# Kernel optimization log

Hardware: AMD Instinct MI355X
Metric: run time of the kernel (lower is better)

The kernel has to match this reference:

```python
import jax, jax.numpy as jnp
import numpy as np

SHAPES = [(100, 100), (50, 50), (25, 25), (13, 13)]
EMBED, HEADS, LEVELS, POINTS = 256, 8, 4, 4
DH = EMBED // HEADS


def setup_inputs() -> dict:
    key = jax.random.key(0)
    ks = jax.random.split(key, 12)
    bs, nq = 4, 10000
    nv = sum(h * w for h, w in SHAPES)
    s = 0.02
    return {
        'query': jax.random.normal(ks[0], (bs, nq, EMBED), jnp.float32),
        'value': jax.random.normal(ks[1], (bs, nv, EMBED), jnp.float32),
        'reference_points': jax.random.uniform(ks[2], (bs, nq, LEVELS, 2), jnp.float32),
        'spatial_shapes': jnp.array(SHAPES, jnp.int32),
        'Wv': s * jax.random.normal(ks[3], (EMBED, EMBED), jnp.float32),
        'bv': jnp.zeros((EMBED,), jnp.float32),
        'Woff': s * jax.random.normal(ks[4], (EMBED, HEADS * LEVELS * POINTS * 2), jnp.float32),
        'boff': s * jax.random.normal(ks[5], (HEADS * LEVELS * POINTS * 2,), jnp.float32),
        'Ww': s * jax.random.normal(ks[6], (EMBED, HEADS * LEVELS * POINTS), jnp.float32),
        'bw': jnp.zeros((HEADS * LEVELS * POINTS,), jnp.float32),
        'Wo': s * jax.random.normal(ks[7], (EMBED, EMBED), jnp.float32),
        'bo': jnp.zeros((EMBED,), jnp.float32),
    }


def _msda(v, loc, aw, bs, nq):
    # v: (bs, nv, heads, dh); loc: (bs, nq, heads, L, P, 2) normalized in [0,1]
    # aw: (bs, nq, heads, L, P). Bilinear grid_sample, align_corners=False, zero padding.
    out = jnp.zeros((bs, HEADS, nq, DH), v.dtype)
    start = 0
    for l, (H, W) in enumerate(SHAPES):
        vl = v[:, start:start + H * W].transpose(0, 2, 1, 3)  # (bs, heads, H*W, dh)
        start += H * W
        locl = loc[:, :, :, l]                                # (bs, nq, heads, P, 2)
        x = locl[..., 0] * W - 0.5                            # align_corners=False mapping
        y = locl[..., 1] * H - 0.5
        x0 = jnp.floor(x); y0 = jnp.floor(y)
        fx = x - x0; fy = y - y0
        x0i = x0.astype(jnp.int32); y0i = y0.astype(jnp.int32)
        sampled = jnp.zeros((bs, HEADS, nq * POINTS, DH), v.dtype)
        for dy, wy in ((0, 1.0 - fy), (1, fy)):
            for dx, wx in ((0, 1.0 - fx), (1, fx)):
                xi = x0i + dx; yi = y0i + dy
                valid = (xi >= 0) & (xi < W) & (yi >= 0) & (yi < H)
                idx = jnp.clip(yi, 0, W and H - 1) * W + jnp.clip(xi, 0, W - 1)
                idx = jnp.clip(yi, 0, H - 1) * W + jnp.clip(xi, 0, W - 1)
                idx_t = idx.transpose(0, 2, 1, 3).reshape(bs, HEADS, nq * POINTS)
                g = jnp.take_along_axis(vl, idx_t[..., None], axis=2)  # (bs,heads,nq*P,dh)
                w = jnp.where(valid, wx * wy, 0.0).transpose(0, 2, 1, 3).reshape(bs, HEADS, -1)
                sampled = sampled + g * w[..., None]
        awl = aw[:, :, :, l].transpose(0, 2, 1, 3).reshape(bs, HEADS, nq * POINTS)
        out = out + (sampled * awl[..., None]).reshape(bs, HEADS, nq, POINTS, DH).sum(3)
    return out.transpose(0, 2, 1, 3).reshape(bs, nq, EMBED)


def reference(query, value, reference_points, spatial_shapes, Wv, bv, Woff, boff, Ww, bw, Wo, bo):
    bs, nq, _ = query.shape
    v = (value @ Wv + bv).reshape(bs, -1, HEADS, DH)
    off = (query @ Woff + boff).reshape(bs, nq, HEADS, LEVELS, POINTS, 2)
    aw = jax.nn.softmax((query @ Ww + bw).reshape(bs, nq, HEADS, LEVELS * POINTS), axis=-1)
    aw = aw.reshape(bs, nq, HEADS, LEVELS, POINTS)
    normalizer = jnp.stack([spatial_shapes[:, 1], spatial_shapes[:, 0]], -1).astype(query.dtype)  # (L,2) = (W,H)
    loc = reference_points[:, :, None, :, None, :] + off / normalizer[None, None, None, :, None, :]
    out = _msda(v, loc, aw, bs, nq)
    out = out @ Wo + bo
    return out + query  # identity residual (dropout in eval mode)
```

## Files before the change

### kernel.cpp

```cpp
#include <hip/hip_runtime.h>
#include <hip/hip_bf16.h>

#define BS     4
#define NQ     10000
#define NV     13294
#define EMBED  256
#define HEADS  8
#define LEVELS 4
#define POINTS 4
#define DH     32

typedef __attribute__((ext_vector_type(8))) short short8;
typedef __attribute__((ext_vector_type(4))) float floatx4;

static __device__ __forceinline__ unsigned short f2b(float f) {
    __hip_bfloat16 h = __float2bfloat16(f);
    return *(unsigned short*)&h;
}

__global__ __launch_bounds__(256) void prep_weights(
    const float* __restrict__ Wv,  const float* __restrict__ Woff,
    const float* __restrict__ boff,const float* __restrict__ Ww,
    const float* __restrict__ bw,  const float* __restrict__ Wo,
    unsigned short* __restrict__ Wvt, unsigned short* __restrict__ Wcatt,
    unsigned short* __restrict__ Wot, float* __restrict__ bcat)
{
    const int n = blockIdx.x;
    const int k = threadIdx.x;
    if (n < 256) {
        Wvt[n * 256 + k] = f2b(Wv[k * 256 + n]);
    } else if (n < 512) {
        Wcatt[(n - 256) * 256 + k] = f2b(Woff[k * 256 + (n - 256)]);
    } else if (n < 640) {
        Wcatt[(n - 256) * 256 + k] = f2b(Ww[k * 128 + (n - 512)]);
    } else {
        Wot[(n - 640) * 256 + k] = f2b(Wo[k * 256 + (n - 640)]);
    }
    if (n == 0) {
        for (int j = k; j < 384; j += 256)
            bcat[j] = (j < 256) ? boff[j] : bw[j - 256];
    }
}

__global__ __launch_bounds__(256) void cast_bf16(
    const float* __restrict__ in, unsigned short* __restrict__ out, int n4)
{
    const int i = blockIdx.x * 256 + threadIdx.x;
    if (i < n4) {
        const float4 f = ((const float4*)in)[i];
        ushort4 o;
        o.x = f2b(f.x); o.y = f2b(f.y); o.z = f2b(f.z); o.w = f2b(f.w);
        ((ushort4*)out)[i] = o;
    }
}

#define ASTR 72

template<int MODE>
__global__ __launch_bounds__(256) void gemm_mfma(
    const unsigned short* __restrict__ A, int M,
    const unsigned short* __restrict__ Bt,
    const float* __restrict__ bias,
    void* __restrict__ Cv, int ldc,
    const float* __restrict__ residual)
{
    __shared__ __align__(16) unsigned short As[128 * ASTR];
    __shared__ __align__(16) unsigned short Bsh[128 * ASTR];

    const int t  = threadIdx.x;
    const int m0 = blockIdx.x * 128;
    const int n0 = blockIdx.y * 128;
    const int K  = 256;

    const int wv   = t >> 6;
    const int lane = t & 63;
    const int wm   = (wv & 1) * 64;
    const int wn   = (wv >> 1) * 64;
    const int lr   = lane & 15;
    const int lk   = (lane >> 4) * 8;

    floatx4 acc[4][4] = {};

    const int ar = t >> 1;
    const int ac = (t & 1) * 32;

    for (int k0 = 0; k0 < K; k0 += 64) {
        uint4 a0 = {}, a1 = {}, a2 = {}, a3 = {};
        const int arow = m0 + ar;
        if (arow < M) {
            const uint4* s = (const uint4*)(A + (size_t)arow * K + k0 + ac);
            a0 = s[0]; a1 = s[1]; a2 = s[2]; a3 = s[3];
        }
        const uint4* bs = (const uint4*)(Bt + (size_t)(n0 + ar) * K + k0 + ac);
        const uint4 b0 = bs[0], b1 = bs[1], b2 = bs[2], b3 = bs[3];

        __syncthreads();
        {
            uint4* ad = (uint4*)&As[ar * ASTR + ac];
            ad[0] = a0; ad[1] = a1; ad[2] = a2; ad[3] = a3;
            uint4* bd = (uint4*)&Bsh[ar * ASTR + ac];
            bd[0] = b0; bd[1] = b1; bd[2] = b2; bd[3] = b3;
        }
        __syncthreads();

        #pragma unroll
        for (int kk = 0; kk < 64; kk += 32) {
            short8 bf[4];
            #pragma unroll
            for (int nt = 0; nt < 4; ++nt)
                bf[nt] = *(const short8*)&Bsh[(wn + nt * 16 + lr) * ASTR + kk + lk];
            #pragma unroll
            for (int mt = 0; mt < 4; ++mt) {
                const short8 af = *(const short8*)&As[(wm + mt * 16 + lr) * ASTR + kk + lk];
                #pragma unroll
                for (int nt = 0; nt < 4; ++nt)
                    acc[mt][nt] = __builtin_amdgcn_mfma_f32_16x16x32_bf16(af, bf[nt], acc[mt][nt], 0, 0, 0);
            }
        }
    }

    const int rbase = m0 + wm + (lane >> 4) * 4;
    #pragma unroll
    for (int nt = 0; nt < 4; ++nt) {
        const int col = n0 + wn + nt * 16 + lr;
        const float bb = bias[col];
        #pragma unroll
        for (int mt = 0; mt < 4; ++mt) {
            #pragma unroll
            for (int r = 0; r < 4; ++r) {
                const int row = rbase + mt * 16 + r;
                if (row < M) {
                    float val = acc[mt][nt][r] + bb;
                    if (MODE == 2) val += residual[(size_t)row * ldc + col];
                    if (MODE == 0)
                        ((unsigned short*)Cv)[(size_t)row * ldc + col] = f2b(val);
                    else
                        ((float*)Cv)[(size_t)row * ldc + col] = val;
                }
            }
        }
    }
}

__global__ __launch_bounds__(256) void msda_sample(
    const unsigned short* __restrict__ v,
    const float* __restrict__ proj,
    const float* __restrict__ rp,
    unsigned short* __restrict__ out)
{
    __shared__ __align__(16) unsigned int taps[4 * 1056];

    const int wave = threadIdx.x >> 6;
    const int lane = threadIdx.x & 63;
    const int q = blockIdx.x * 4 + wave;
    const int b = blockIdx.y;
    const int rowq = b * NQ + q;
    const float* prow = proj + (size_t)rowq * 384;

    const int hA = lane >> 3;
    const int li = lane & 7;
    const int c0 = li * 2;

    const float2 lg = *(const float2*)&prow[256 + hA * 16 + c0];
    float mx = fmaxf(lg.x, lg.y);
    mx = fmaxf(mx, __shfl_xor(mx, 1));
    mx = fmaxf(mx, __shfl_xor(mx, 2));
    mx = fmaxf(mx, __shfl_xor(mx, 4));
    const float e0 = __expf(lg.x - mx);
    const float e1 = __expf(lg.y - mx);
    float ssum = e0 + e1;
    ssum += __shfl_xor(ssum, 1);
    ssum += __shfl_xor(ssum, 2);
    ssum += __shfl_xor(ssum, 4);
    const float inv = 1.0f / ssum;

    const int l = c0 >> 2;
    const int Wl = (l == 0) ? 100 : (l == 1) ? 50 : (l == 2) ? 25 : 13;
    const int st = (l == 0) ? 0 : (l == 1) ? 10000 : (l == 2) ? 12500 : 13125;
    const int Hl = Wl;
    const float fW = (float)Wl, fH = (float)Hl;

    const float2 rxy = *(const float2*)&rp[((size_t)rowq * 4 + l) * 2];

    unsigned int* tbase = taps + wave * 1056 + hA * 132;

    #pragma unroll
    for (int cc = 0; cc < 2; ++cc) {
        const int c = c0 + cc;
        const float2 oxy = *(const float2*)&prow[hA * 32 + c * 2];
        const float aww = (cc ? e1 : e0) * inv;
        const float x = fmaf(rxy.x, fW, oxy.x) - 0.5f;
        const float y = fmaf(rxy.y, fH, oxy.y) - 0.5f;
        const float x0f = floorf(x), y0f = floorf(y);
        const float fx = x - x0f, fy = y - y0f;
        const int ix = (int)x0f, iy = (int)y0f;
        const float wxv[2] = {1.f - fx, fx};
        const float wyv[2] = {1.f - fy, fy};

        uint4 ent[2];
        #pragma unroll
        for (int tp = 0; tp < 4; ++tp) {
            const int dy = tp >> 1, dx = tp & 1;
            const int xi = ix + dx, yi = iy + dy;
            const bool ok = (xi >= 0) && (xi < Wl) && (yi >= 0) && (yi < Hl);
            const int cx = min(max(xi, 0), Wl - 1);
            const int cy = min(max(yi, 0), Hl - 1);
            const unsigned int off = (unsigned int)(st + cy * Wl + cx) * 512u + (unsigned int)hA * 64u;
            const float w = ok ? wyv[dy] * wxv[dx] * aww : 0.f;
            ((unsigned int*)&ent[tp >> 1])[(tp & 1) * 2 + 0] = off;
            ((unsigned int*)&ent[tp >> 1])[(tp & 1) * 2 + 1] = __float_as_uint(w);
        }
        *(uint4*)&tbase[(c * 4 + 0) * 2] = ent[0];
        *(uint4*)&tbase[(c * 4 + 2) * 2] = ent[1];
    }

    __syncthreads();

    const int h = lane >> 3;
    const unsigned int lane_off = (unsigned int)(lane & 7) * 8u;
    const char* vb = (const char*)v + (size_t)b * NV * 512 + lane_off;
    const uint4* tp4 = (const uint4*)(taps + wave * 1056 + h * 132);

    float a0 = 0.f, a1 = 0.f, a2 = 0.f, a3 = 0.f;
    #pragma unroll 8
    for (int j = 0; j < 32; ++j) {
        const uint4 ee = tp4[j];
        const uint2 g0 = *(const uint2*)(vb + ee.x);
        const uint2 g1 = *(const uint2*)(vb + ee.z);
        const float w0 = __uint_as_float(ee.y);
        const float w1 = __uint_as_float(ee.w);
        a0 = fmaf(w0, __uint_as_float(g0.x << 16), a0);
        a1 = fmaf(w0, __uint_as_float(g0.x & 0xFFFF0000u), a1);
        a2 = fmaf(w0, __uint_as_float(g0.y << 16), a2);
        a3 = fmaf(w0, __uint_as_float(g0.y & 0xFFFF0000u), a3);
        a0 = fmaf(w1, __uint_as_float(g1.x << 16), a0);
        a1 = fmaf(w1, __uint_as_float(g1.x & 0xFFFF0000u), a1);
        a2 = fmaf(w1, __uint_as_float(g1.y << 16), a2);
        a3 = fmaf(w1, __uint_as_float(g1.y & 0xFFFF0000u), a3);
    }

    ushort4 o;
    o.x = f2b(a0); o.y = f2b(a1); o.z = f2b(a2); o.w = f2b(a3);
    *(ushort4*)&out[(size_t)rowq * 256 + h * 32 + (lane & 7) * 4] = o;
}

extern "C" void kernel_launch(void* const* d_in, const int* in_sizes, int n_in,
                              void* d_out, int out_size, void* d_ws, size_t ws_size,
                              hipStream_t stream) {
    const float* query = (const float*)d_in[0];
    const float* value = (const float*)d_in[1];
    const float* rp    = (const float*)d_in[2];
    const float* Wv    = (const float*)d_in[4];
    const float* bv    = (const float*)d_in[5];
    const float* Woff  = (const float*)d_in[6];
    const float* boff  = (const float*)d_in[7];
    const float* Ww    = (const float*)d_in[8];
    const float* bw    = (const float*)d_in[9];
    const float* Wo    = (const float*)d_in[10];
    const float* bo    = (const float*)d_in[11];
    float* out = (float*)d_out;

    const int Mv = BS * NV;
    const int Mq = BS * NQ;

    char* ws = (char*)d_ws;
    const size_t SZ_A    = (size_t)Mv * 256 * 2;
    const size_t SZ_V    = (size_t)Mv * 256 * 2;
    const size_t SZ_PROJ = (size_t)Mq * 384 * 4;
    const size_t SZ_QB   = (size_t)Mq * 256 * 2;
    unsigned short* bufA  = (unsigned short*)(ws);
    unsigned short* v_bf  = (unsigned short*)(ws + SZ_A);
    float*          proj  = (float*)(ws + SZ_A + SZ_V);
    unsigned short* q_bf  = (unsigned short*)(ws + SZ_A + SZ_V + SZ_PROJ);
    char* wp = ws + SZ_A + SZ_V + SZ_PROJ + SZ_QB;
    unsigned short* Wvt   = (unsigned short*)(wp);
    unsigned short* Wcatt = (unsigned short*)(wp + 256 * 256 * 2);
    unsigned short* Wot   = (unsigned short*)(wp + 256 * 256 * 2 + 384 * 256 * 2);
    float*          bcat  = (float*)(wp + 256 * 256 * 2 + 384 * 256 * 2 + 256 * 256 * 2);

    prep_weights<<<896, 256, 0, stream>>>(Wv, Woff, boff, Ww, bw, Wo, Wvt, Wcatt, Wot, bcat);
    cast_bf16<<<(Mv * 64 + 255) / 256, 256, 0, stream>>>(value, bufA, Mv * 64);
    cast_bf16<<<(Mq * 64 + 255) / 256, 256, 0, stream>>>(query, q_bf, Mq * 64);

    gemm_mfma<0><<<dim3((Mv + 127) / 128, 2), 256, 0, stream>>>(
        bufA, Mv, Wvt, bv, v_bf, 256, nullptr);

    gemm_mfma<1><<<dim3((Mq + 127) / 128, 3), 256, 0, stream>>>(
        q_bf, Mq, Wcatt, bcat, proj, 384, nullptr);

    msda_sample<<<dim3(NQ / 4, BS), 256, 0, stream>>>(v_bf, proj, rp, bufA);

    gemm_mfma<2><<<dim3((Mq + 127) / 128, 2), 256, 0, stream>>>(
        bufA, Mq, Wot, bo, out, 256, query);
}
```

Measured before the change: 341.0 us.

## Fuse input casts into GEMM loads, merge value and query projections into one launch

```diff
diff --git a/kernel.cpp b/kernel.cpp
--- a/kernel.cpp
+++ b/kernel.cpp
@@ -16,6 +16,13 @@
 static __device__ __forceinline__ unsigned short f2b(float f) {
     __hip_bfloat16 h = __float2bfloat16(f);
     return *(unsigned short*)&h;
+}
+static __device__ __forceinline__ float b2f(unsigned short u) {
+    return __uint_as_float(((unsigned int)u) << 16);
+}
+static __device__ __forceinline__ unsigned int pk_bf16(float x, float y) {
+    __hip_bfloat162 h = __float22bfloat162_rn(make_float2(x, y));
+    unsigned int u; __builtin_memcpy(&u, &h, 4); return u;
 }
 
 __global__ __launch_bounds__(256) void prep_weights(
@@ -42,34 +49,21 @@
     }
 }
 
-__global__ __launch_bounds__(256) void cast_bf16(
-    const float* __restrict__ in, unsigned short* __restrict__ out, int n4)
-{
-    const int i = blockIdx.x * 256 + threadIdx.x;
-    if (i < n4) {
-        const float4 f = ((const float4*)in)[i];
-        ushort4 o;
-        o.x = f2b(f.x); o.y = f2b(f.y); o.z = f2b(f.z); o.w = f2b(f.w);
-        ((ushort4*)out)[i] = o;
-    }
-}
-
 #define ASTR 72
 
-template<int MODE>
-__global__ __launch_bounds__(256) void gemm_mfma(
-    const unsigned short* __restrict__ A, int M,
+template<int MODE, bool AF32>
+static __device__ __forceinline__ void gemm_body(
+    unsigned short* As, unsigned short* Bsh,
+    const void* __restrict__ Aptr, int M,
     const unsigned short* __restrict__ Bt,
     const float* __restrict__ bias,
     void* __restrict__ Cv, int ldc,
-    const float* __restrict__ residual)
-{
-    __shared__ __align__(16) unsigned short As[128 * ASTR];
-    __shared__ __align__(16) unsigned short Bsh[128 * ASTR];
-
+    const float* __restrict__ residual,
+    int mb, int nb)
+{
     const int t  = threadIdx.x;
-    const int m0 = blockIdx.x * 128;
-    const int n0 = blockIdx.y * 128;
+    const int m0 = mb * 128;
+    const int n0 = nb * 128;
     const int K  = 256;
 
     const int wv   = t >> 6;
@@ -85,11 +79,25 @@
     const int ac = (t & 1) * 32;
 
     for (int k0 = 0; k0 < K; k0 += 64) {
-        uint4 a0 = {}, a1 = {}, a2 = {}, a3 = {};
+        uint4 a[4] = {{}, {}, {}, {}};
         const int arow = m0 + ar;
-        if (arow < M) {
-            const uint4* s = (const uint4*)(A + (size_t)arow * K + k0 + ac);
-            a0 = s[0]; a1 = s[1]; a2 = s[2]; a3 = s[3];
+        if (AF32) {
+            if (arow < M) {
+                const float4* s = (const float4*)((const float*)Aptr + (size_t)arow * K + k0 + ac);
+                #pragma unroll
+                for (int i = 0; i < 4; ++i) {
+                    const float4 f0 = s[2 * i], f1 = s[2 * i + 1];
+                    a[i].x = pk_bf16(f0.x, f0.y);
+                    a[i].y = pk_bf16(f0.z, f0.w);
+                    a[i].z = pk_bf16(f1.x, f1.y);
+                    a[i].w = pk_bf16(f1.z, f1.w);
+                }
+            }
+        } else {
+            if (arow < M) {
+                const uint4* s = (const uint4*)((const unsigned short*)Aptr + (size_t)arow * K + k0 + ac);
+                a[0] = s[0]; a[1] = s[1]; a[2] = s[2]; a[3] = s[3];
+            }
         }
         const uint4* bs = (const uint4*)(Bt + (size_t)(n0 + ar) * K + k0 + ac);
         const uint4 b0 = bs[0], b1 = bs[1], b2 = bs[2], b3 = bs[3];
@@ -97,7 +105,7 @@
         __syncthreads();
         {
             uint4* ad = (uint4*)&As[ar * ASTR + ac];
-            ad[0] = a0; ad[1] = a1; ad[2] = a2; ad[3] = a3;
+            ad[0] = a[0]; ad[1] = a[1]; ad[2] = a[2]; ad[3] = a[3];
             uint4* bd = (uint4*)&Bsh[ar * ASTR + ac];
             bd[0] = b0; bd[1] = b1; bd[2] = b2; bd[3] = b3;
         }
@@ -142,9 +150,39 @@
     }
 }
 
+__global__ __launch_bounds__(256) void gemm_fused12(
+    const float* __restrict__ value, const float* __restrict__ query,
+    const unsigned short* __restrict__ Wvt, const unsigned short* __restrict__ Wcatt,
+    const float* __restrict__ bv, const float* __restrict__ bcat,
+    unsigned short* __restrict__ vout, unsigned short* __restrict__ projout)
+{
+    __shared__ __align__(16) unsigned short As[128 * ASTR];
+    __shared__ __align__(16) unsigned short Bsh[128 * ASTR];
+    const unsigned int bid = blockIdx.x;
+    if (bid < 832u) {
+        gemm_body<0, true>(As, Bsh, value, BS * NV, Wvt, bv, vout, 256, nullptr,
+                           (int)(bid >> 1), (int)(bid & 1));
+    } else {
+        const unsigned int b2 = bid - 832u;
+        gemm_body<0, true>(As, Bsh, query, BS * NQ, Wcatt, bcat, projout, 384, nullptr,
+                           (int)(b2 / 3u), (int)(b2 % 3u));
+    }
+}
+
+__global__ __launch_bounds__(256) void gemm_out(
+    const unsigned short* __restrict__ msda, const unsigned short* __restrict__ Wot,
+    const float* __restrict__ bo, float* __restrict__ out,
+    const float* __restrict__ query)
+{
+    __shared__ __align__(16) unsigned short As[128 * ASTR];
+    __shared__ __align__(16) unsigned short Bsh[128 * ASTR];
+    gemm_body<2, false>(As, Bsh, msda, BS * NQ, Wot, bo, out, 256, query,
+                        (int)blockIdx.x, (int)blockIdx.y);
+}
+
 __global__ __launch_bounds__(256) void msda_sample(
     const unsigned short* __restrict__ v,
-    const float* __restrict__ proj,
+    const unsigned short* __restrict__ proj,
     const float* __restrict__ rp,
     unsigned short* __restrict__ out)
 {
@@ -155,19 +193,20 @@
     const int q = blockIdx.x * 4 + wave;
     const int b = blockIdx.y;
     const int rowq = b * NQ + q;
-    const float* prow = proj + (size_t)rowq * 384;
+    const unsigned short* prow = proj + (size_t)rowq * 384;
 
     const int hA = lane >> 3;
     const int li = lane & 7;
     const int c0 = li * 2;
 
-    const float2 lg = *(const float2*)&prow[256 + hA * 16 + c0];
-    float mx = fmaxf(lg.x, lg.y);
+    const ushort2 lgu = *(const ushort2*)&prow[256 + hA * 16 + c0];
+    const float lgx = b2f(lgu.x), lgy = b2f(lgu.y);
+    float mx = fmaxf(lgx, lgy);
     mx = fmaxf(mx, __shfl_xor(mx, 1));
     mx = fmaxf(mx, __shfl_xor(mx, 2));
     mx = fmaxf(mx, __shfl_xor(mx, 4));
-    const float e0 = __expf(lg.x - mx);
-    const float e1 = __expf(lg.y - mx);
+    const float e0 = __expf(lgx - mx);
+    const float e1 = __expf(lgy - mx);
     float ssum = e0 + e1;
     ssum += __shfl_xor(ssum, 1);
     ssum += __shfl_xor(ssum, 2);
@@ -187,10 +226,11 @@
     #pragma unroll
     for (int cc = 0; cc < 2; ++cc) {
         const int c = c0 + cc;
-        const float2 oxy = *(const float2*)&prow[hA * 32 + c * 2];
+        const ushort2 oxyu = *(const ushort2*)&prow[hA * 32 + c * 2];
+        const float ox = b2f(oxyu.x), oy = b2f(oxyu.y);
         const float aww = (cc ? e1 : e0) * inv;
-        const float x = fmaf(rxy.x, fW, oxy.x) - 0.5f;
-        const float y = fmaf(rxy.y, fH, oxy.y) - 0.5f;
+        const float x = fmaf(rxy.x, fW, ox) - 0.5f;
+        const float y = fmaf(rxy.y, fH, oy) - 0.5f;
         const float x0f = floorf(x), y0f = floorf(y);
         const float fx = x - x0f, fy = y - y0f;
         const int ix = (int)x0f, iy = (int)y0f;
@@ -218,15 +258,15 @@
 
     const int h = lane >> 3;
     const unsigned int lane_off = (unsigned int)(lane & 7) * 8u;
-    const char* vb = (const char*)v + (size_t)b * NV * 512 + lane_off;
+    const char* vbase = (const char*)v + (size_t)b * NV * 512;
     const uint4* tp4 = (const uint4*)(taps + wave * 1056 + h * 132);
 
     float a0 = 0.f, a1 = 0.f, a2 = 0.f, a3 = 0.f;
     #pragma unroll 8
     for (int j = 0; j < 32; ++j) {
         const uint4 ee = tp4[j];
-        const uint2 g0 = *(const uint2*)(vb + ee.x);
-        const uint2 g1 = *(const uint2*)(vb + ee.z);
+        const uint2 g0 = *(const uint2*)(vbase + (ee.x + lane_off));
+        const uint2 g1 = *(const uint2*)(vbase + (ee.z + lane_off));
         const float w0 = __uint_as_float(ee.y);
         const float w1 = __uint_as_float(ee.w);
         a0 = fmaf(w0, __uint_as_float(g0.x << 16), a0);
@@ -264,32 +304,24 @@
     const int Mq = BS * NQ;
 
     char* ws = (char*)d_ws;
-    const size_t SZ_A    = (size_t)Mv * 256 * 2;
+    const size_t SZ_MSDA = (size_t)Mq * 256 * 2;
     const size_t SZ_V    = (size_t)Mv * 256 * 2;
-    const size_t SZ_PROJ = (size_t)Mq * 384 * 4;
-    const size_t SZ_QB   = (size_t)Mq * 256 * 2;
-    unsigned short* bufA  = (unsigned short*)(ws);
-    unsigned short* v_bf  = (unsigned short*)(ws + SZ_A);
-    float*          proj  = (float*)(ws + SZ_A + SZ_V);
-    unsigned short* q_bf  = (unsigned short*)(ws + SZ_A + SZ_V + SZ_PROJ);
-    char* wp = ws + SZ_A + SZ_V + SZ_PROJ + SZ_QB;
+    const size_t SZ_PROJ = (size_t)Mq * 384 * 2;
+    unsigned short* msda  = (unsigned short*)(ws);
+    unsigned short* v_bf  = (unsigned short*)(ws + SZ_MSDA);
+    unsigned short* proj  = (unsigned short*)(ws + SZ_MSDA + SZ_V);
+    char* wp = ws + SZ_MSDA + SZ_V + SZ_PROJ;
     unsigned short* Wvt   = (unsigned short*)(wp);
     unsigned short* Wcatt = (unsigned short*)(wp + 256 * 256 * 2);
     unsigned short* Wot   = (unsigned short*)(wp + 256 * 256 * 2 + 384 * 256 * 2);
     float*          bcat  = (float*)(wp + 256 * 256 * 2 + 384 * 256 * 2 + 256 * 256 * 2);
 
     prep_weights<<<896, 256, 0, stream>>>(Wv, Woff, boff, Ww, bw, Wo, Wvt, Wcatt, Wot, bcat);
-    cast_bf16<<<(Mv * 64 + 255) / 256, 256, 0, stream>>>(value, bufA, Mv * 64);
-    cast_bf16<<<(Mq * 64 + 255) / 256, 256, 0, stream>>>(query, q_bf, Mq * 64);
-
-    gemm_mfma<0><<<dim3((Mv + 127) / 128, 2), 256, 0, stream>>>(
-        bufA, Mv, Wvt, bv, v_bf, 256, nullptr);
-
-    gemm_mfma<1><<<dim3((Mq + 127) / 128, 3), 256, 0, stream>>>(
-        q_bf, Mq, Wcatt, bcat, proj, 384, nullptr);
-
-    msda_sample<<<dim3(NQ / 4, BS), 256, 0, stream>>>(v_bf, proj, rp, bufA);
-
-    gemm_mfma<2><<<dim3((Mq + 127) / 128, 2), 256, 0, stream>>>(
-        bufA, Mq, Wot, bo, out, 256, query);
-}
+
+    gemm_fused12<<<832 + 939, 256, 0, stream>>>(
+        value, query, Wvt, Wcatt, bv, bcat, v_bf, proj);
+
+    msda_sample<<<dim3(NQ / 4, BS), 256, 0, stream>>>(v_bf, proj, rp, msda);
+
+    gemm_out<<<dim3((Mq + 127) / 128, 2), 256, 0, stream>>>(msda, Wot, bo, out, query);
+}
```

Result: faster. 332.7 us (-2.4%).
